# Performance work log

Measured on AMD Instinct MI355X. Metric: run time of the kernel, lower is better.

The kernel has to match this reference:

```python
import jax, jax.numpy as jnp
import numpy as np

B, T, C, DD = 32, 2048, 32, 8  # batch, time steps, value channels, demo channels


def setup_inputs() -> dict:
    key = jax.random.key(0)
    k1, k2, k3, k4 = jax.random.split(key, 4)
    demo = jax.random.normal(k1, (B, DD), dtype=jnp.float32)
    times = jax.random.uniform(k2, (B, T), dtype=jnp.float32)
    values = jax.random.normal(k3, (B, T, C), dtype=jnp.float32)
    measurements = jax.random.randint(k4, (B, T, C), 0, 2) > 0
    return {"demo": demo, "times": times, "values": values, "measurements": measurements}


def reference(demo, times, values, measurements):
    # Faithful dense-packed version of the TF per-channel ragged pack:
    # for each channel c, observed (time, one_hot(c), value) triples are packed
    # to the front of each batch row (tf.where + stable sort on batch id keeps
    # within-row time order); rows with zero observations get one all-zero pad
    # entry (csd = -1 -> one_hot gives zeros), which dense zero-padding subsumes.
    b, t, c = values.shape
    dd = demo.shape[-1]
    depth = dd + c          # one-hot depth, as in build()
    F = depth + 2           # [time, one_hot(depth), value]
    dt = values.dtype

    mask = measurements
    maskf = mask.astype(dt)
    # packed position of each observed (b, t, c) within its (b, c) row
    pos = jnp.cumsum(mask.astype(jnp.int32), axis=1) - 1          # [B,T,C]
    pos_safe = jnp.where(mask, pos, t)                            # dump slot t

    onehot_c = jnp.eye(depth, dtype=dt)[:c]                       # [C, depth]
    feat = jnp.concatenate([
        (times[:, :, None] * maskf)[..., None],                   # time  [B,T,C,1]
        maskf[..., None] * onehot_c[None, None],                  # csd   [B,T,C,depth]
        (values * maskf)[..., None],                              # value [B,T,C,1]
    ], axis=-1)                                                   # [B,T,C,F]

    cI = jnp.broadcast_to(jnp.arange(c)[None, None, :], (b, t, c))
    bI = jnp.broadcast_to(jnp.arange(b)[:, None, None], (b, t, c))
    out = jnp.zeros((c, b, t + 1, F), dtype=dt)
    out = out.at[cI, bI, pos_safe].add(feat)                      # unique except dump
    packed = out[:, :, :t]                                        # [C,B,T,F]

    # demo channels: one entry per row, time=0, one_hot index = C + x - 1 (as in source)
    idx = c + jnp.arange(dd) - 1                                  # [DD]
    oh = jnp.eye(depth, dtype=dt)[idx]                            # [DD, depth]
    demo_row = jnp.concatenate([
        jnp.zeros((dd, b, 1), dtype=dt),                          # time = 0
        jnp.broadcast_to(oh[:, None, :], (dd, b, depth)),         # one-hot
        demo.T[..., None],                                        # value
    ], axis=-1)                                                   # [DD,B,F]
    demo_full = jnp.zeros((dd, b, t, F), dtype=dt).at[:, :, 0, :].set(demo_row)

    return jnp.concatenate([packed, demo_full], axis=0)           # [C+DD,B,T,F]
```

## Files before the change

### kernel.cpp

```cpp
#include <hip/hip_runtime.h>
#include <stdint.h>

#define BB 32
#define TT 2048
#define CC 32
#define DDIM 8
#define FF 42
#define NCH (CC + DDIM)
#define SLAB_B (TT * FF)
#define SLAB_CH (BB * SLAB_B)
#define TOTAL (40L * SLAB_CH)

__device__ __forceinline__ int detect_mask_mode(const void* meas) {
    const unsigned* w = (const unsigned*)meas;
    unsigned A = 0, Aodd = 0;
    for (int i = 0; i < 256; ++i) A |= w[i];
    for (int i = 1; i < 256; i += 2) Aodd |= w[i];
    unsigned hi = A >> 24;
    if (hi == 0u) return (Aodd == 0u) ? 3 : 0;
    if (hi >= 0x3Cu && hi <= 0x3Fu) return (A & 0xFFFFu) ? 2 : 0;
    return 1;
}

__device__ __forceinline__ int read_mask(const void* meas, size_t idx, int mode) {
    if (mode == 3) return ((const unsigned long long*)meas)[idx] != 0ull;
    if (mode == 1) return ((const uint8_t*)meas)[idx] != 0;
    if (mode == 2) return ((const unsigned short*)meas)[idx] != 0;
    return ((const unsigned*)meas)[idx] != 0u;
}

__global__ void compact_kernel(const float* __restrict__ demo,
                               const float* __restrict__ times,
                               const float* __restrict__ values,
                               const void* __restrict__ meas,
                               float* __restrict__ ws_time,
                               float* __restrict__ ws_val,
                               int* __restrict__ count,
                               float* __restrict__ ws_demo) {
    __shared__ int s_mode;
    if (threadIdx.x == 0) s_mode = detect_mask_mode(meas);
    __syncthreads();
    const int mode = s_mode;

    if (blockIdx.x == 0 && threadIdx.x < BB * DDIM)
        ws_demo[threadIdx.x] = demo[threadIdx.x];

    int wid = (int)((blockIdx.x * blockDim.x + threadIdx.x) >> 6);
    int lane = (int)(threadIdx.x & 63);
    if (wid >= BB * CC) return;
    int b = wid / CC, c = wid % CC;

    float* wt = ws_time + (size_t)(c * BB + b) * TT;
    float* wv = ws_val + (size_t)(c * BB + b) * TT;

    int kbase = 0;
    for (int t0 = 0; t0 < TT; t0 += 64) {
        int t = t0 + lane;
        size_t idx = (size_t)(b * TT + t) * CC + c;
        int m = read_mask(meas, idx, mode);
        unsigned long long bits = __ballot(m);
        if (m) {
            int pos = kbase + __popcll(bits & ((1ull << lane) - 1ull));
            wt[pos] = times[(size_t)b * TT + t];
            wv[pos] = values[idx];
        }
        kbase += __popcll(bits);
    }
    if (lane == 0) count[c * BB + b] = kbase;
}

template <bool HASWS>
__global__ void fill_kernel(const float* __restrict__ ws_demo,
                            const float* __restrict__ demo_raw,
                            const float* __restrict__ ws_time,
                            const float* __restrict__ ws_val,
                            const int* __restrict__ count,
                            float* __restrict__ out) {
    unsigned g = blockIdx.x * 256u + threadIdx.x;
    if (g >= (unsigned)(TOTAL / 4)) return;
    unsigned j = g * 4u;
    unsigned ch = j / (unsigned)SLAB_CH;
    unsigned r = j - ch * (unsigned)SLAB_CH;
    unsigned b = r / (unsigned)SLAB_B;
    unsigned q = r - b * (unsigned)SLAB_B;
    int k = (int)(q / (unsigned)FF);
    int f = (int)(q - (unsigned)k * FF);

    float o[4];
    if (ch < CC) {
        int cnt = HASWS ? count[ch * BB + b] : 0;
        const float* wt = ws_time + (size_t)(ch * BB + b) * TT;
        const float* wv = ws_val + (size_t)(ch * BB + b) * TT;
        int onef = 1 + (int)ch;
#pragma unroll
        for (int s = 0; s < 4; ++s) {
            float v = 0.0f;
            if (k < cnt) {
                if (f == 0) v = wt[k];
                else if (f == onef) v = 1.0f;
                else if (f == 41) v = wv[k];
            }
            o[s] = v;
            if (++f == FF) { f = 0; ++k; }
        }
    } else {
        int d = (int)ch - CC;
        float dv = HASWS ? ws_demo[b * DDIM + d] : demo_raw[(size_t)b * DDIM + d];
#pragma unroll
        for (int s = 0; s < 4; ++s) {
            float v = 0.0f;
            if (k == 0) {
                if (f == 32 + d) v = 1.0f;
                else if (f == 41) v = dv;
            }
            o[s] = v;
            if (++f == FF) { f = 0; ++k; }
        }
    }
    float4 pack = make_float4(o[0], o[1], o[2], o[3]);
    reinterpret_cast<float4*>(out)[g] = pack;
}

__global__ void scatter_kernel(const float* __restrict__ times,
                               const float* __restrict__ values,
                               const void* __restrict__ meas,
                               float* __restrict__ out) {
    __shared__ int s_mode;
    if (threadIdx.x == 0) s_mode = detect_mask_mode(meas);
    __syncthreads();
    const int mode = s_mode;

    int wid = (int)((blockIdx.x * blockDim.x + threadIdx.x) >> 6);
    int lane = (int)(threadIdx.x & 63);
    if (wid >= BB * CC) return;
    int b = wid / CC, c = wid % CC;

    float* base = out + (size_t)(c * BB + b) * SLAB_B;

    int kbase = 0;
    for (int t0 = 0; t0 < TT; t0 += 64) {
        int t = t0 + lane;
        size_t idx = (size_t)(b * TT + t) * CC + c;
        int m = read_mask(meas, idx, mode);
        unsigned long long bits = __ballot(m);
        if (m) {
            int pos = kbase + __popcll(bits & ((1ull << lane) - 1ull));
            float* row = base + (size_t)pos * FF;
            row[0] = times[(size_t)b * TT + t];
            row[1 + c] = 1.0f;
            row[41] = values[idx];
        }
        kbase += __popcll(bits);
    }
}

extern "C" void kernel_launch(void* const* d_in, const int* in_sizes, int n_in,
                              void* d_out, int out_size, void* d_ws, size_t ws_size,
                              hipStream_t stream) {
    const float* demo   = (const float*)d_in[0];
    const float* times  = (const float*)d_in[1];
    const float* values = (const float*)d_in[2];
    const void*  meas   = d_in[3];
    float* out = (float*)d_out;

    const size_t n_cb = (size_t)CC * BB;
    const size_t ws_need = 2 * n_cb * TT * sizeof(float)
                         + n_cb * sizeof(int)
                         + (size_t)BB * DDIM * sizeof(float);
    const long ngroups = TOTAL / 4;
    const int fill_blocks = (int)((ngroups + 255) / 256);
    const int scan_blocks = (BB * CC * 64 + 255) / 256;

    if (ws_size >= ws_need) {
        float* ws_time = (float*)d_ws;
        float* ws_val  = ws_time + n_cb * TT;
        int* count     = (int*)(ws_val + n_cb * TT);
        float* ws_demo = (float*)(count + n_cb);
        compact_kernel<<<scan_blocks, 256, 0, stream>>>(demo, times, values, meas,
                                                        ws_time, ws_val, count, ws_demo);
        fill_kernel<true><<<fill_blocks, 256, 0, stream>>>(ws_demo, nullptr,
                                                           ws_time, ws_val, count, out);
    } else {
        fill_kernel<false><<<fill_blocks, 256, 0, stream>>>(nullptr, demo,
                                                            nullptr, nullptr, nullptr, out);
        scatter_kernel<<<scan_blocks, 256, 0, stream>>>(times, values, meas, out);
    }
}
```

Baseline: 483.9 us.

## Parallelize compaction per row across 8 waves and widen fill stores

The compaction kernel now gives each (channel, batch) row its own 512-thread block. Eight waves each count their 256-step slice, combine offsets through shared memory, then scatter, replacing one wave walking the whole row serially. Mask-mode detection becomes a parallel atomicOr over the block instead of a single-thread 256-word loop. The fill kernel writes eight floats per thread as two float4 stores, halving the thread count, which may raise register use per thread.

```diff
diff --git a/kernel.cpp b/kernel.cpp
--- a/kernel.cpp
+++ b/kernel.cpp
@@ -6,21 +6,9 @@
 #define CC 32
 #define DDIM 8
 #define FF 42
-#define NCH (CC + DDIM)
 #define SLAB_B (TT * FF)
 #define SLAB_CH (BB * SLAB_B)
 #define TOTAL (40L * SLAB_CH)
-
-__device__ __forceinline__ int detect_mask_mode(const void* meas) {
-    const unsigned* w = (const unsigned*)meas;
-    unsigned A = 0, Aodd = 0;
-    for (int i = 0; i < 256; ++i) A |= w[i];
-    for (int i = 1; i < 256; i += 2) Aodd |= w[i];
-    unsigned hi = A >> 24;
-    if (hi == 0u) return (Aodd == 0u) ? 3 : 0;
-    if (hi >= 0x3Cu && hi <= 0x3Fu) return (A & 0xFFFFu) ? 2 : 0;
-    return 1;
-}
 
 __device__ __forceinline__ int read_mask(const void* meas, size_t idx, int mode) {
     if (mode == 3) return ((const unsigned long long*)meas)[idx] != 0ull;
@@ -29,33 +17,72 @@
     return ((const unsigned*)meas)[idx] != 0u;
 }
 
-__global__ void compact_kernel(const float* __restrict__ demo,
-                               const float* __restrict__ times,
-                               const float* __restrict__ values,
-                               const void* __restrict__ meas,
-                               float* __restrict__ ws_time,
-                               float* __restrict__ ws_val,
-                               int* __restrict__ count,
-                               float* __restrict__ ws_demo) {
-    __shared__ int s_mode;
-    if (threadIdx.x == 0) s_mode = detect_mask_mode(meas);
+__device__ __forceinline__ int block_detect_mask_mode(const void* meas,
+                                                      unsigned* s_A, unsigned* s_Aodd) {
+    if (threadIdx.x == 0) { *s_A = 0u; *s_Aodd = 0u; }
     __syncthreads();
-    const int mode = s_mode;
-
-    if (blockIdx.x == 0 && threadIdx.x < BB * DDIM)
+    if (threadIdx.x < 256) {
+        unsigned w = ((const unsigned*)meas)[threadIdx.x];
+        atomicOr(s_A, w);
+        if (threadIdx.x & 1) atomicOr(s_Aodd, w);
+    }
+    __syncthreads();
+    unsigned A = *s_A, Aodd = *s_Aodd;
+    unsigned hi = A >> 24;
+    if (hi == 0u) return (Aodd == 0u) ? 3 : 0;
+    if (hi >= 0x3Cu && hi <= 0x3Fu) return (A & 0xFFFFu) ? 2 : 0;
+    return 1;
+}
+
+__global__ __launch_bounds__(512)
+void compact_kernel(const float* __restrict__ demo,
+                    const float* __restrict__ times,
+                    const float* __restrict__ values,
+                    const void* __restrict__ meas,
+                    float* __restrict__ ws_time,
+                    float* __restrict__ ws_val,
+                    int* __restrict__ count,
+                    float* __restrict__ ws_demo) {
+    __shared__ unsigned s_A, s_Aodd;
+    __shared__ int s_wcnt[8];
+    const int mode = block_detect_mask_mode(meas, &s_A, &s_Aodd);
+
+    const int bid = blockIdx.x;
+    const int c = bid >> 5, b = bid & 31;
+    const int w = threadIdx.x >> 6;
+    const int lane = threadIdx.x & 63;
+    const int tbase = w * 256;
+
+    if (bid == 0 && threadIdx.x < BB * DDIM)
         ws_demo[threadIdx.x] = demo[threadIdx.x];
 
-    int wid = (int)((blockIdx.x * blockDim.x + threadIdx.x) >> 6);
-    int lane = (int)(threadIdx.x & 63);
-    if (wid >= BB * CC) return;
-    int b = wid / CC, c = wid % CC;
-
-    float* wt = ws_time + (size_t)(c * BB + b) * TT;
-    float* wv = ws_val + (size_t)(c * BB + b) * TT;
-
-    int kbase = 0;
-    for (int t0 = 0; t0 < TT; t0 += 64) {
-        int t = t0 + lane;
+    int mycnt = 0;
+#pragma unroll
+    for (int i = 0; i < 4; ++i) {
+        int t = tbase + i * 64 + lane;
+        size_t idx = (size_t)(b * TT + t) * CC + c;
+        mycnt += __popcll(__ballot(read_mask(meas, idx, mode)));
+    }
+    if (lane == 0) s_wcnt[w] = mycnt;
+    __syncthreads();
+
+    int base = 0;
+#pragma unroll
+    for (int i = 0; i < 8; ++i) if (i < w) base += s_wcnt[i];
+    if (threadIdx.x == 0) {
+        int tot = 0;
+#pragma unroll
+        for (int i = 0; i < 8; ++i) tot += s_wcnt[i];
+        count[bid] = tot;
+    }
+
+    float* wt = ws_time + (size_t)bid * TT;
+    float* wv = ws_val + (size_t)bid * TT;
+
+    int kbase = base;
+#pragma unroll
+    for (int i = 0; i < 4; ++i) {
+        int t = tbase + i * 64 + lane;
         size_t idx = (size_t)(b * TT + t) * CC + c;
         int m = read_mask(meas, idx, mode);
         unsigned long long bits = __ballot(m);
@@ -66,19 +93,19 @@
         }
         kbase += __popcll(bits);
     }
-    if (lane == 0) count[c * BB + b] = kbase;
 }
 
 template <bool HASWS>
-__global__ void fill_kernel(const float* __restrict__ ws_demo,
-                            const float* __restrict__ demo_raw,
-                            const float* __restrict__ ws_time,
-                            const float* __restrict__ ws_val,
-                            const int* __restrict__ count,
-                            float* __restrict__ out) {
+__global__ __launch_bounds__(256)
+void fill_kernel(const float* __restrict__ ws_demo,
+                 const float* __restrict__ demo_raw,
+                 const float* __restrict__ ws_time,
+                 const float* __restrict__ ws_val,
+                 const int* __restrict__ count,
+                 float* __restrict__ out) {
     unsigned g = blockIdx.x * 256u + threadIdx.x;
-    if (g >= (unsigned)(TOTAL / 4)) return;
-    unsigned j = g * 4u;
+    if (g >= (unsigned)(TOTAL / 8)) return;
+    unsigned j = g * 8u;
     unsigned ch = j / (unsigned)SLAB_CH;
     unsigned r = j - ch * (unsigned)SLAB_CH;
     unsigned b = r / (unsigned)SLAB_B;
@@ -86,14 +113,14 @@
     int k = (int)(q / (unsigned)FF);
     int f = (int)(q - (unsigned)k * FF);
 
-    float o[4];
+    float o[8];
     if (ch < CC) {
         int cnt = HASWS ? count[ch * BB + b] : 0;
         const float* wt = ws_time + (size_t)(ch * BB + b) * TT;
         const float* wv = ws_val + (size_t)(ch * BB + b) * TT;
         int onef = 1 + (int)ch;
 #pragma unroll
-        for (int s = 0; s < 4; ++s) {
+        for (int s = 0; s < 8; ++s) {
             float v = 0.0f;
             if (k < cnt) {
                 if (f == 0) v = wt[k];
@@ -107,7 +134,7 @@
         int d = (int)ch - CC;
         float dv = HASWS ? ws_demo[b * DDIM + d] : demo_raw[(size_t)b * DDIM + d];
 #pragma unroll
-        for (int s = 0; s < 4; ++s) {
+        for (int s = 0; s < 8; ++s) {
             float v = 0.0f;
             if (k == 0) {
                 if (f == 32 + d) v = 1.0f;
@@ -117,18 +144,17 @@
             if (++f == FF) { f = 0; ++k; }
         }
     }
-    float4 pack = make_float4(o[0], o[1], o[2], o[3]);
-    reinterpret_cast<float4*>(out)[g] = pack;
+    float4* dst = reinterpret_cast<float4*>(out) + (size_t)g * 2;
+    dst[0] = make_float4(o[0], o[1], o[2], o[3]);
+    dst[1] = make_float4(o[4], o[5], o[6], o[7]);
 }
 
 __global__ void scatter_kernel(const float* __restrict__ times,
                                const float* __restrict__ values,
                                const void* __restrict__ meas,
                                float* __restrict__ out) {
-    __shared__ int s_mode;
-    if (threadIdx.x == 0) s_mode = detect_mask_mode(meas);
-    __syncthreads();
-    const int mode = s_mode;
+    __shared__ unsigned s_A, s_Aodd;
+    const int mode = block_detect_mask_mode(meas, &s_A, &s_Aodd);
 
     int wid = (int)((blockIdx.x * blockDim.x + threadIdx.x) >> 6);
     int lane = (int)(threadIdx.x & 63);
@@ -167,8 +193,7 @@
     const size_t ws_need = 2 * n_cb * TT * sizeof(float)
                          + n_cb * sizeof(int)
                          + (size_t)BB * DDIM * sizeof(float);
-    const long ngroups = TOTAL / 4;
-    const int fill_blocks = (int)((ngroups + 255) / 256);
+    const int fill_blocks = (int)(TOTAL / 8 / 256);
     const int scan_blocks = (BB * CC * 64 + 255) / 256;
 
     if (ws_size >= ws_need) {
@@ -176,8 +201,8 @@
         float* ws_val  = ws_time + n_cb * TT;
         int* count     = (int*)(ws_val + n_cb * TT);
         float* ws_demo = (float*)(count + n_cb);
-        compact_kernel<<<scan_blocks, 256, 0, stream>>>(demo, times, values, meas,
-                                                        ws_time, ws_val, count, ws_demo);
+        compact_kernel<<<BB * CC, 512, 0, stream>>>(demo, times, values, meas,
+                                                    ws_time, ws_val, count, ws_demo);
         fill_kernel<true><<<fill_blocks, 256, 0, stream>>>(ws_demo, nullptr,
                                                            ws_time, ws_val, count, out);
     } else {
```

Result: faster. 470.4 us (-2.8%).
